# Kernel tuning notes

Measured on AMD Instinct MI355X. Metric: run time of the kernel, lower is better.

The kernel has to match this reference:

```python
import jax, jax.numpy as jnp
import numpy as np

B = 65536
NUM_INPUTS = 256
NUM_HIDDEN = 256


def setup_inputs() -> dict:
    key = jax.random.key(0)
    ks = jax.random.split(key, 11)
    f32 = jnp.float32
    return {
        "x": jax.random.normal(ks[0], (B, NUM_INPUTS), dtype=f32),
        "h_t_1": jax.random.normal(ks[1], (B, NUM_HIDDEN), dtype=f32),
        "Wz": jax.random.normal(ks[2], (NUM_INPUTS, NUM_HIDDEN), dtype=f32),
        "Uz": jax.random.normal(ks[3], (NUM_HIDDEN, NUM_HIDDEN), dtype=f32),
        "bz": jax.random.normal(ks[4], (NUM_HIDDEN,), dtype=f32),
        "Wr": jax.random.normal(ks[5], (NUM_INPUTS, NUM_HIDDEN), dtype=f32),
        "Ur": jax.random.normal(ks[6], (NUM_HIDDEN, NUM_HIDDEN), dtype=f32),
        "br": jax.random.normal(ks[7], (NUM_HIDDEN,), dtype=f32),
        "Wh": jax.random.normal(ks[8], (NUM_INPUTS, NUM_HIDDEN), dtype=f32),
        "Uh": jax.random.normal(ks[9], (NUM_HIDDEN, NUM_HIDDEN), dtype=f32),
        "bh": jax.random.normal(ks[10], (NUM_HIDDEN,), dtype=f32),
    }


def reference(x, h_t_1, Wz, Uz, bz, Wr, Ur, br, Wh, Uh, bh):
    # update gate z = sigmoid(x@Wz + h@Uz + bz)
    z = jax.nn.sigmoid(x @ Wz + h_t_1 @ Uz + bz)
    # reset gate r = sigmoid(x@Wr + h@Ur + br)
    r = jax.nn.sigmoid(x @ Wr + h_t_1 @ Ur + br)
    # candidate: tanh(x@Wh + (r*h)@Uh + bh)
    h_hat = jnp.tanh(x @ Wh + (r * h_t_1) @ Uh + bh)
    h_t = z * h_t_1 + (1.0 - z) * h_hat
    return (h_t, h_t)
```

## Files before the change

kernel.cpp:

```cpp
#include <hip/hip_runtime.h>
#include <hip/hip_fp16.h>


#define NHID 256
#define B_ROWS 65536
#define MT 64
#define RT 4
#define CPW 2
#define GATE_STRIDE (16 * 16 * 64 * 8)

typedef _Float16 half8 __attribute__((ext_vector_type(8)));
typedef _Float16 half4_t __attribute__((ext_vector_type(4)));
typedef _Float16 half2_t __attribute__((ext_vector_type(2)));
typedef float floatx4 __attribute__((ext_vector_type(4)));

__device__ __forceinline__ int lidx(int m, int c) {
    return m * 256 + ((((c >> 3) ^ (m & 7)) << 3)) + (c & 7);
}

__global__ __launch_bounds__(256) void pack_weights_kernel(
    const float* __restrict__ Wz, const float* __restrict__ Uz,
    const float* __restrict__ Wr, const float* __restrict__ Ur,
    const float* __restrict__ Wh, const float* __restrict__ Uh,
    _Float16* __restrict__ packed)
{
    int tid = blockIdx.x * blockDim.x + threadIdx.x;
    int lane = tid & 63;
    int s    = (tid >> 6) & 15;
    int ct   = (tid >> 10) & 15;
    int g    = tid >> 14;
    const float* W = (g == 0) ? Wz : (g == 1) ? Wr : Wh;
    const float* U = (g == 0) ? Uz : (g == 1) ? Ur : Uh;
    int n  = ct * 16 + (lane & 15);
    int k0 = s * 32 + (lane >> 4) * 8;
    half8 v;
#pragma unroll
    for (int j = 0; j < 8; ++j) {
        int k = k0 + j;
        float f = (k < 256) ? W[k * 256 + n] : U[(k - 256) * 256 + n];
        v[j] = (_Float16)f;
    }
    *reinterpret_cast<half8*>(packed + (size_t)tid * 8) = v;
}

__global__ __launch_bounds__(512, 2) void gru_main_kernel(
    const float* __restrict__ x, const float* __restrict__ h,
    const _Float16* __restrict__ wpack,
    const float* __restrict__ bz, const float* __restrict__ br,
    const float* __restrict__ bh,
    float* __restrict__ out)
{
    __shared__ __align__(16) unsigned char smem[MT * 260 * 4];
    _Float16* lx = reinterpret_cast<_Float16*>(smem);
    _Float16* lh = lx + MT * 256;
    float* lout = reinterpret_cast<float*>(smem);

    const int tid  = threadIdx.x;
    const int lane = tid & 63;
    const int wave = tid >> 6;
    const int row0 = blockIdx.x * MT;
    const int m_lo = lane & 15;
    const int quad = lane >> 4;

    {
        const float4* xv = reinterpret_cast<const float4*>(x + (size_t)row0 * NHID);
        const float4* hv = reinterpret_cast<const float4*>(h + (size_t)row0 * NHID);
#pragma unroll
        for (int it = 0; it < (MT * 64) / 512; ++it) {
            int i = it * 512 + tid;
            int m = i >> 6;
            int c = (i & 63) * 4;
            float4 a = xv[i];
            float4 b = hv[i];
            half4_t va = { (_Float16)a.x, (_Float16)a.y, (_Float16)a.z, (_Float16)a.w };
            half4_t vb = { (_Float16)b.x, (_Float16)b.y, (_Float16)b.z, (_Float16)b.w };
            *reinterpret_cast<half4_t*>(&lx[lidx(m, c)]) = va;
            *reinterpret_cast<half4_t*>(&lh[lidx(m, c)]) = vb;
        }
    }
    __syncthreads();

    const _Float16* wz = wpack;
    const _Float16* wr = wpack + GATE_STRIDE;
    const _Float16* wh = wpack + 2 * GATE_STRIDE;

    const int mx = m_lo & 7;

    half2_t zpk[CPW][RT][4];

    {
        floatx4 accz[CPW][RT];
        floatx4 accr[CPW][RT];
#pragma unroll
        for (int c = 0; c < CPW; ++c)
#pragma unroll
            for (int rt = 0; rt < RT; ++rt) {
                accz[c][rt] = (floatx4){0.f, 0.f, 0.f, 0.f};
                accr[c][rt] = (floatx4){0.f, 0.f, 0.f, 0.f};
            }

#pragma unroll
        for (int s = 0; s < 16; ++s) {
            const _Float16* asrc = (s < 8) ? lx : lh;
            const int kcx = (((s & 7) * 4 + quad) ^ mx) << 3;
            half8 af[RT];
#pragma unroll
            for (int rt = 0; rt < RT; ++rt)
                af[rt] = *reinterpret_cast<const half8*>(&asrc[(rt * 16 + m_lo) * 256 + kcx]);
#pragma unroll
            for (int c = 0; c < CPW; ++c) {
                const int ct = wave * CPW + c;
                half8 bzf = *reinterpret_cast<const half8*>(&wz[(size_t)((ct * 16 + s) * 64 + lane) * 8]);
                half8 brf = *reinterpret_cast<const half8*>(&wr[(size_t)((ct * 16 + s) * 64 + lane) * 8]);
#pragma unroll
                for (int rt = 0; rt < RT; ++rt) {
                    accz[c][rt] = __builtin_amdgcn_mfma_f32_16x16x32_f16(af[rt], bzf, accz[c][rt], 0, 0, 0);
                    accr[c][rt] = __builtin_amdgcn_mfma_f32_16x16x32_f16(af[rt], brf, accr[c][rt], 0, 0, 0);
                }
            }
        }

        __syncthreads();

#pragma unroll
        for (int c = 0; c < CPW; ++c) {
            const int col = (wave * CPW + c) * 16 + m_lo;
            const float bzv = bz[col];
            const float brv = br[col];
#pragma unroll
            for (int rt = 0; rt < RT; ++rt) {
#pragma unroll
                for (int e = 0; e < 4; ++e) {
                    const int row = rt * 16 + quad * 4 + e;
                    float sz = accz[c][rt][e] + bzv;
                    float sr = accr[c][rt][e] + brv;
                    float zv = 1.f / (1.f + __expf(-sz));
                    float rv = 1.f / (1.f + __expf(-sr));
                    const int li = lidx(row, col);
                    float hval = (float)lh[li];
                    lh[li] = (_Float16)(rv * hval);
                    zpk[c][rt][e] = half2_t{ (_Float16)(zv * hval), (_Float16)(1.f - zv) };
                }
            }
        }
    }
    __syncthreads();

    floatx4 acch[CPW][RT];
#pragma unroll
    for (int c = 0; c < CPW; ++c)
#pragma unroll
        for (int rt = 0; rt < RT; ++rt)
            acch[c][rt] = (floatx4){0.f, 0.f, 0.f, 0.f};

#pragma unroll
    for (int s = 0; s < 16; ++s) {
        const _Float16* asrc = (s < 8) ? lx : lh;
        const int kcx = (((s & 7) * 4 + quad) ^ mx) << 3;
        half8 af[RT];
#pragma unroll
        for (int rt = 0; rt < RT; ++rt)
            af[rt] = *reinterpret_cast<const half8*>(&asrc[(rt * 16 + m_lo) * 256 + kcx]);
#pragma unroll
        for (int c = 0; c < CPW; ++c) {
            const int ct = wave * CPW + c;
            half8 bhf = *reinterpret_cast<const half8*>(&wh[(size_t)((ct * 16 + s) * 64 + lane) * 8]);
#pragma unroll
            for (int rt = 0; rt < RT; ++rt)
                acch[c][rt] = __builtin_amdgcn_mfma_f32_16x16x32_f16(af[rt], bhf, acch[c][rt], 0, 0, 0);
        }
    }
    __syncthreads();

#pragma unroll
    for (int c = 0; c < CPW; ++c) {
        const int col = (wave * CPW + c) * 16 + m_lo;
        const float bhv = bh[col];
#pragma unroll
        for (int rt = 0; rt < RT; ++rt) {
#pragma unroll
            for (int e = 0; e < 4; ++e) {
                const int row = rt * 16 + quad * 4 + e;
                float sh = acch[c][rt][e] + bhv;
                float e2 = __expf(2.f * sh);
                float hh = 1.f - 2.f / (e2 + 1.f);
                float zh  = (float)zpk[c][rt][e][0];
                float omz = (float)zpk[c][rt][e][1];
                lout[row * 260 + col] = zh + omz * hh;
            }
        }
    }
    __syncthreads();

    const size_t OUT2 = (size_t)B_ROWS * NHID;
#pragma unroll
    for (int it = 0; it < (MT * 64) / 512; ++it) {
        int i = it * 512 + tid;
        int m = i >> 6;
        int cv = (i & 63) * 4;
        float4 v = *reinterpret_cast<const float4*>(&lout[m * 260 + cv]);
        size_t idx = (size_t)(row0 + m) * NHID + cv;
        *reinterpret_cast<float4*>(&out[idx]) = v;
        *reinterpret_cast<float4*>(&out[OUT2 + idx]) = v;
    }
}

extern "C" void kernel_launch(void* const* d_in, const int* in_sizes, int n_in,
                              void* d_out, int out_size, void* d_ws, size_t ws_size,
                              hipStream_t stream) {
    (void)in_sizes; (void)n_in; (void)out_size; (void)ws_size;
    const float* x  = (const float*)d_in[0];
    const float* h  = (const float*)d_in[1];
    const float* Wz = (const float*)d_in[2];
    const float* Uz = (const float*)d_in[3];
    const float* bz = (const float*)d_in[4];
    const float* Wr = (const float*)d_in[5];
    const float* Ur = (const float*)d_in[6];
    const float* br = (const float*)d_in[7];
    const float* Wh = (const float*)d_in[8];
    const float* Uh = (const float*)d_in[9];
    const float* bh = (const float*)d_in[10];
    float* out = (float*)d_out;
    _Float16* wpack = (_Float16*)d_ws;

    pack_weights_kernel<<<192, 256, 0, stream>>>(Wz, Uz, Wr, Ur, Wh, Uh, wpack);
    gru_main_kernel<<<B_ROWS / MT, 512, 0, stream>>>(x, h, wpack, bz, br, bh, out);
}
```

Baseline: 326.0 us.

## Prefetch weight fragments, raise occupancy, and store output directly from registers

Double-buffers the per-step weight fragment loads from global memory so the next k-step's fragments arrive while the current MFMAs run, and issues the first fragments before the activation staging. LDS drops from the padded output-staging size to exactly the x/h tiles, launch bounds ask for 4 blocks per CU, and bias loads are hoisted. The LDS output staging and one barrier are removed; results go straight from accumulators to global memory as scalar nontemporal stores. Barriers become raw s_barrier with explicit lgkm waits and setprio around MFMA bursts. The risks are register pressure under the tighter launch bound, and scattered 4-byte stores (16 adjacent lanes per row) replacing coalesced float4 writes.

```diff
diff --git a/kernel.cpp b/kernel.cpp
--- a/kernel.cpp
+++ b/kernel.cpp
@@ -16,6 +16,13 @@
 
 __device__ __forceinline__ int lidx(int m, int c) {
     return m * 256 + ((((c >> 3) ^ (m & 7)) << 3)) + (c & 7);
+}
+
+__device__ __forceinline__ void barrier_lgkm() {
+    __builtin_amdgcn_sched_barrier(0);
+    asm volatile("s_waitcnt lgkmcnt(0)" ::: "memory");
+    __builtin_amdgcn_s_barrier();
+    __builtin_amdgcn_sched_barrier(0);
 }
 
 __global__ __launch_bounds__(256) void pack_weights_kernel(
@@ -43,17 +50,19 @@
     *reinterpret_cast<half8*>(packed + (size_t)tid * 8) = v;
 }
 
-__global__ __launch_bounds__(512, 2) void gru_main_kernel(
+#define WFRAG(base, ct, s) \
+    (*reinterpret_cast<const half8*>((base) + (size_t)((((ct) * 16 + (s)) * 64 + lane) * 8)))
+
+__global__ __launch_bounds__(512, 4) void gru_main_kernel(
     const float* __restrict__ x, const float* __restrict__ h,
     const _Float16* __restrict__ wpack,
     const float* __restrict__ bz, const float* __restrict__ br,
     const float* __restrict__ bh,
     float* __restrict__ out)
 {
-    __shared__ __align__(16) unsigned char smem[MT * 260 * 4];
-    _Float16* lx = reinterpret_cast<_Float16*>(smem);
-    _Float16* lh = lx + MT * 256;
-    float* lout = reinterpret_cast<float*>(smem);
+    __shared__ __align__(16) _Float16 lsm[MT * 256 * 2];
+    _Float16* lx = lsm;
+    _Float16* lh = lsm + MT * 256;
 
     const int tid  = threadIdx.x;
     const int lane = tid & 63;
@@ -61,6 +70,18 @@
     const int row0 = blockIdx.x * MT;
     const int m_lo = lane & 15;
     const int quad = lane >> 4;
+    const int mx   = m_lo & 7;
+    const int ct0  = wave * CPW;
+
+    const _Float16* wz = wpack;
+    const _Float16* wr = wpack + GATE_STRIDE;
+    const _Float16* wh = wpack + 2 * GATE_STRIDE;
+
+    half8 wzb[2][CPW], wrb[2][CPW];
+    wzb[0][0] = WFRAG(wz, ct0 + 0, 0);
+    wzb[0][1] = WFRAG(wz, ct0 + 1, 0);
+    wrb[0][0] = WFRAG(wr, ct0 + 0, 0);
+    wrb[0][1] = WFRAG(wr, ct0 + 1, 0);
 
     {
         const float4* xv = reinterpret_cast<const float4*>(x + (size_t)row0 * NHID);
@@ -78,130 +99,131 @@
             *reinterpret_cast<half4_t*>(&lh[lidx(m, c)]) = vb;
         }
     }
-    __syncthreads();
-
-    const _Float16* wz = wpack;
-    const _Float16* wr = wpack + GATE_STRIDE;
-    const _Float16* wh = wpack + 2 * GATE_STRIDE;
-
-    const int mx = m_lo & 7;
+    barrier_lgkm();
 
     half2_t zpk[CPW][RT][4];
 
-    {
-        floatx4 accz[CPW][RT];
-        floatx4 accr[CPW][RT];
-#pragma unroll
-        for (int c = 0; c < CPW; ++c)
-#pragma unroll
-            for (int rt = 0; rt < RT; ++rt) {
-                accz[c][rt] = (floatx4){0.f, 0.f, 0.f, 0.f};
-                accr[c][rt] = (floatx4){0.f, 0.f, 0.f, 0.f};
-            }
-
-#pragma unroll
-        for (int s = 0; s < 16; ++s) {
-            const _Float16* asrc = (s < 8) ? lx : lh;
-            const int kcx = (((s & 7) * 4 + quad) ^ mx) << 3;
-            half8 af[RT];
-#pragma unroll
-            for (int rt = 0; rt < RT; ++rt)
-                af[rt] = *reinterpret_cast<const half8*>(&asrc[(rt * 16 + m_lo) * 256 + kcx]);
-#pragma unroll
-            for (int c = 0; c < CPW; ++c) {
-                const int ct = wave * CPW + c;
-                half8 bzf = *reinterpret_cast<const half8*>(&wz[(size_t)((ct * 16 + s) * 64 + lane) * 8]);
-                half8 brf = *reinterpret_cast<const half8*>(&wr[(size_t)((ct * 16 + s) * 64 + lane) * 8]);
-#pragma unroll
-                for (int rt = 0; rt < RT; ++rt) {
-                    accz[c][rt] = __builtin_amdgcn_mfma_f32_16x16x32_f16(af[rt], bzf, accz[c][rt], 0, 0, 0);
-                    accr[c][rt] = __builtin_amdgcn_mfma_f32_16x16x32_f16(af[rt], brf, accr[c][rt], 0, 0, 0);
-                }
-            }
-        }
-
-        __syncthreads();
-
-#pragma unroll
-        for (int c = 0; c < CPW; ++c) {
-            const int col = (wave * CPW + c) * 16 + m_lo;
-            const float bzv = bz[col];
-            const float brv = br[col];
-#pragma unroll
-            for (int rt = 0; rt < RT; ++rt) {
-#pragma unroll
-                for (int e = 0; e < 4; ++e) {
-                    const int row = rt * 16 + quad * 4 + e;
-                    float sz = accz[c][rt][e] + bzv;
-                    float sr = accr[c][rt][e] + brv;
-                    float zv = 1.f / (1.f + __expf(-sz));
-                    float rv = 1.f / (1.f + __expf(-sr));
-                    const int li = lidx(row, col);
-                    float hval = (float)lh[li];
-                    lh[li] = (_Float16)(rv * hval);
-                    zpk[c][rt][e] = half2_t{ (_Float16)(zv * hval), (_Float16)(1.f - zv) };
-                }
-            }
-        }
-    }
-    __syncthreads();
-
-    floatx4 acch[CPW][RT];
+    floatx4 accz[CPW][RT];
+    floatx4 accr[CPW][RT];
 #pragma unroll
     for (int c = 0; c < CPW; ++c)
 #pragma unroll
-        for (int rt = 0; rt < RT; ++rt)
-            acch[c][rt] = (floatx4){0.f, 0.f, 0.f, 0.f};
+        for (int rt = 0; rt < RT; ++rt) {
+            accz[c][rt] = (floatx4){0.f, 0.f, 0.f, 0.f};
+            accr[c][rt] = (floatx4){0.f, 0.f, 0.f, 0.f};
+        }
 
 #pragma unroll
     for (int s = 0; s < 16; ++s) {
+        const int cur = s & 1, nxt = cur ^ 1;
+        if (s < 15) {
+            wzb[nxt][0] = WFRAG(wz, ct0 + 0, s + 1);
+            wzb[nxt][1] = WFRAG(wz, ct0 + 1, s + 1);
+            wrb[nxt][0] = WFRAG(wr, ct0 + 0, s + 1);
+            wrb[nxt][1] = WFRAG(wr, ct0 + 1, s + 1);
+        }
         const _Float16* asrc = (s < 8) ? lx : lh;
         const int kcx = (((s & 7) * 4 + quad) ^ mx) << 3;
         half8 af[RT];
 #pragma unroll
         for (int rt = 0; rt < RT; ++rt)
             af[rt] = *reinterpret_cast<const half8*>(&asrc[(rt * 16 + m_lo) * 256 + kcx]);
-#pragma unroll
-        for (int c = 0; c < CPW; ++c) {
-            const int ct = wave * CPW + c;
-            half8 bhf = *reinterpret_cast<const half8*>(&wh[(size_t)((ct * 16 + s) * 64 + lane) * 8]);
-#pragma unroll
-            for (int rt = 0; rt < RT; ++rt)
-                acch[c][rt] = __builtin_amdgcn_mfma_f32_16x16x32_f16(af[rt], bhf, acch[c][rt], 0, 0, 0);
-        }
-    }
-    __syncthreads();
-
+        __builtin_amdgcn_s_setprio(1);
+#pragma unroll
+        for (int c = 0; c < CPW; ++c)
+#pragma unroll
+            for (int rt = 0; rt < RT; ++rt) {
+                accz[c][rt] = __builtin_amdgcn_mfma_f32_16x16x32_f16(af[rt], wzb[cur][c], accz[c][rt], 0, 0, 0);
+                accr[c][rt] = __builtin_amdgcn_mfma_f32_16x16x32_f16(af[rt], wrb[cur][c], accr[c][rt], 0, 0, 0);
+            }
+        __builtin_amdgcn_s_setprio(0);
+    }
+
+    half8 whb[2][CPW];
+    whb[0][0] = WFRAG(wh, ct0 + 0, 0);
+    whb[0][1] = WFRAG(wh, ct0 + 1, 0);
+    float bzv[CPW], brv[CPW], bhv[CPW];
 #pragma unroll
     for (int c = 0; c < CPW; ++c) {
-        const int col = (wave * CPW + c) * 16 + m_lo;
-        const float bhv = bh[col];
+        const int col = (ct0 + c) * 16 + m_lo;
+        bzv[c] = bz[col];
+        brv[c] = br[col];
+        bhv[c] = bh[col];
+    }
+
+    barrier_lgkm();
+
+#pragma unroll
+    for (int c = 0; c < CPW; ++c) {
+        const int col = (ct0 + c) * 16 + m_lo;
 #pragma unroll
         for (int rt = 0; rt < RT; ++rt) {
 #pragma unroll
             for (int e = 0; e < 4; ++e) {
                 const int row = rt * 16 + quad * 4 + e;
-                float sh = acch[c][rt][e] + bhv;
+                float sz = accz[c][rt][e] + bzv[c];
+                float sr = accr[c][rt][e] + brv[c];
+                float zv = 1.f / (1.f + __expf(-sz));
+                float rv = 1.f / (1.f + __expf(-sr));
+                const int li = lidx(row, col);
+                float hval = (float)lh[li];
+                lh[li] = (_Float16)(rv * hval);
+                zpk[c][rt][e] = half2_t{ (_Float16)(zv * hval), (_Float16)(1.f - zv) };
+            }
+        }
+    }
+
+    barrier_lgkm();
+
+    floatx4 acch[CPW][RT];
+#pragma unroll
+    for (int c = 0; c < CPW; ++c)
+#pragma unroll
+        for (int rt = 0; rt < RT; ++rt)
+            acch[c][rt] = (floatx4){0.f, 0.f, 0.f, 0.f};
+
+#pragma unroll
+    for (int s = 0; s < 16; ++s) {
+        const int cur = s & 1, nxt = cur ^ 1;
+        if (s < 15) {
+            whb[nxt][0] = WFRAG(wh, ct0 + 0, s + 1);
+            whb[nxt][1] = WFRAG(wh, ct0 + 1, s + 1);
+        }
+        const _Float16* asrc = (s < 8) ? lx : lh;
+        const int kcx = (((s & 7) * 4 + quad) ^ mx) << 3;
+        half8 af[RT];
+#pragma unroll
+        for (int rt = 0; rt < RT; ++rt)
+            af[rt] = *reinterpret_cast<const half8*>(&asrc[(rt * 16 + m_lo) * 256 + kcx]);
+        __builtin_amdgcn_s_setprio(1);
+#pragma unroll
+        for (int c = 0; c < CPW; ++c)
+#pragma unroll
+            for (int rt = 0; rt < RT; ++rt)
+                acch[c][rt] = __builtin_amdgcn_mfma_f32_16x16x32_f16(af[rt], whb[cur][c], acch[c][rt], 0, 0, 0);
+        __builtin_amdgcn_s_setprio(0);
+    }
+
+    const size_t OUT2 = (size_t)B_ROWS * NHID;
+#pragma unroll
+    for (int c = 0; c < CPW; ++c) {
+        const int col = (ct0 + c) * 16 + m_lo;
+#pragma unroll
+        for (int rt = 0; rt < RT; ++rt) {
+#pragma unroll
+            for (int e = 0; e < 4; ++e) {
+                const int row = rt * 16 + quad * 4 + e;
+                float sh = acch[c][rt][e] + bhv[c];
                 float e2 = __expf(2.f * sh);
                 float hh = 1.f - 2.f / (e2 + 1.f);
                 float zh  = (float)zpk[c][rt][e][0];
                 float omz = (float)zpk[c][rt][e][1];
-                lout[row * 260 + col] = zh + omz * hh;
+                float ht  = zh + omz * hh;
+                size_t idx = (size_t)(row0 + row) * NHID + col;
+                __builtin_nontemporal_store(ht, &out[idx]);
+                __builtin_nontemporal_store(ht, &out[OUT2 + idx]);
             }
         }
-    }
-    __syncthreads();
-
-    const size_t OUT2 = (size_t)B_ROWS * NHID;
-#pragma unroll
-    for (int it = 0; it < (MT * 64) / 512; ++it) {
-        int i = it * 512 + tid;
-        int m = i >> 6;
-        int cv = (i & 63) * 4;
-        float4 v = *reinterpret_cast<const float4*>(&lout[m * 260 + cv]);
-        size_t idx = (size_t)(row0 + m) * NHID + cv;
-        *reinterpret_cast<float4*>(&out[idx]) = v;
-        *reinterpret_cast<float4*>(&out[OUT2 + idx]) = v;
     }
 }
 
```

After: 319.6 us. 1.02x faster.
